# Optimization experiments

Measured on AMD Instinct MI355X. Metric: run time of the kernel, lower is better.

Reference implementation:

```python
import jax, jax.numpy as jnp
import numpy as np

T, B, E, H = 2048, 2, 1024, 16
HD = E // H
EPS = 1e-5


def setup_inputs() -> dict:
    key = jax.random.key(0)
    k1, k2, k3 = jax.random.split(key, 3)
    bound_in = float(np.sqrt(6.0 / (3 * E + E)))   # xavier_uniform for [3E,E]
    bound_out = float(np.sqrt(6.0 / (E + E)))      # xavier_uniform for [E,E]
    return {
        "query": jax.random.normal(k1, (T, B, E), dtype=jnp.float32),
        "gamma": jnp.ones((E,), dtype=jnp.float32),
        "beta": jnp.zeros((E,), dtype=jnp.float32),
        "in_proj_weight": jax.random.uniform(k2, (3 * E, E), jnp.float32, -bound_in, bound_in),
        "out_proj_weight": jax.random.uniform(k3, (E, E), jnp.float32, -bound_out, bound_out),
    }


def reference(query, gamma, beta, in_proj_weight, out_proj_weight):
    # LayerNorm over channel dim
    mean = jnp.mean(query, axis=-1, keepdims=True)
    var = jnp.mean(jnp.square(query - mean), axis=-1, keepdims=True)
    ln = (query - mean) * jax.lax.rsqrt(var + EPS) * gamma + beta  # [T,B,E]

    # Fused QKV projection (no bias): qkv = ln @ W^T, W: [3E, E]
    qkv = jnp.einsum("tbe,fe->tbf", ln, in_proj_weight)  # [T,B,3E]
    q, k, v = jnp.split(qkv, 3, axis=-1)
    q = q.reshape(T, B, H, HD) * (HD ** -0.5)
    k = k.reshape(T, B, H, HD)
    v = v.reshape(T, B, H, HD)

    # Attention: scores [B,H,T,T]
    scores = jnp.einsum("tbhd,sbhd->bhts", q, k)
    attn = jax.nn.softmax(scores, axis=-1)
    ctx = jnp.einsum("bhts,sbhd->tbhd", attn, v).reshape(T, B, E)

    # Output projection + residual add (dropout prob = 0)
    out = jnp.einsum("tbe,fe->tbf", ctx, out_proj_weight)
    return query + out
```

## Files before the change

kernel.cpp:

```cpp
#include <hip/hip_runtime.h>
#include <hip/hip_bf16.h>
#include <math.h>

#define T_DIM 2048
#define B_DIM 2
#define E_DIM 1024
#define H_DIM 16
#define HD_DIM 64
#define M_DIM (T_DIM * B_DIM)
#define BH_DIM (B_DIM * H_DIM)

using bf16x8 = __attribute__((ext_vector_type(8))) __bf16;
using u16x8  = __attribute__((ext_vector_type(8))) unsigned short;
using f32x4  = __attribute__((ext_vector_type(4))) float;

static __device__ __forceinline__ unsigned short f2bf(float f) {
  unsigned u = __builtin_bit_cast(unsigned, f);
  u += 0x7fff + ((u >> 16) & 1);
  return (unsigned short)(u >> 16);
}

__device__ __forceinline__ void gload_lds16(const void* g, void* l) {
  __builtin_amdgcn_global_load_lds(
      (const __attribute__((address_space(1))) unsigned int*)g,
      (__attribute__((address_space(3))) unsigned int*)l, 16, 0, 0);
}

__global__ __launch_bounds__(256) void prep_kernel(
    const float* __restrict__ q, const float* __restrict__ gamma,
    const float* __restrict__ beta, unsigned short* __restrict__ ln_out,
    const float* __restrict__ w1, unsigned short* __restrict__ o1, int n1,
    const float* __restrict__ w2, unsigned short* __restrict__ o2, int n2) {
  int blk = blockIdx.x;
  int tid = threadIdx.x;
  if (blk >= M_DIM) {
    int i = (blk - M_DIM) * 256 + tid;
    const float* in; unsigned short* out; int idx;
    if (i < n1) { in = w1; out = o1; idx = i; }
    else if (i < n1 + n2) { in = w2; out = o2; idx = i - n1; }
    else return;
    float4 v = ((const float4*)in)[idx];
    ushort4 o;
    o.x = f2bf(v.x); o.y = f2bf(v.y); o.z = f2bf(v.z); o.w = f2bf(v.w);
    ((ushort4*)out)[idx] = o;
    return;
  }
  int row = blk;
  const float4* qr = (const float4*)(q + (size_t)row * E_DIM);
  float4 x = qr[tid];
  float s  = x.x + x.y + x.z + x.w;
  float ss = x.x * x.x + x.y * x.y + x.z * x.z + x.w * x.w;
#pragma unroll
  for (int off = 32; off >= 1; off >>= 1) {
    s  += __shfl_xor(s, off, 64);
    ss += __shfl_xor(ss, off, 64);
  }
  __shared__ float red[8];
  int wid = tid >> 6, lane = tid & 63;
  if (lane == 0) { red[wid] = s; red[4 + wid] = ss; }
  __syncthreads();
  s  = red[0] + red[1] + red[2] + red[3];
  ss = red[4] + red[5] + red[6] + red[7];
  float mean = s * (1.0f / E_DIM);
  float var  = ss * (1.0f / E_DIM) - mean * mean;
  float rstd = rsqrtf(var + 1e-5f);
  float4 g4 = ((const float4*)gamma)[tid];
  float4 b4 = ((const float4*)beta)[tid];
  ushort4 o;
  o.x = f2bf((x.x - mean) * rstd * g4.x + b4.x);
  o.y = f2bf((x.y - mean) * rstd * g4.y + b4.y);
  o.z = f2bf((x.z - mean) * rstd * g4.z + b4.z);
  o.w = f2bf((x.w - mean) * rstd * g4.w + b4.w);
  ((ushort4*)(ln_out + (size_t)row * E_DIM))[tid] = o;
}

__global__ __launch_bounds__(256) void gemm0_kernel(
    const unsigned short* __restrict__ A, const unsigned short* __restrict__ Bw,
    unsigned short* __restrict__ out_qkv) {
  __shared__ alignas(16) unsigned short lA[3][128 * 32];
  __shared__ alignas(16) unsigned short lB[3][128 * 32];
  int tid = threadIdx.x;
  int wid = tid >> 6, lane = tid & 63;
  int wm = wid >> 1, wn = wid & 1;
  int g = lane >> 4, lr = lane & 15;
  int m0 = blockIdx.y * 128, n0 = blockIdx.x * 128;
  f32x4 acc[4][4] = {};

  int srcRow[2], srcCol[2];
#pragma unroll
  for (int c = 0; c < 2; ++c) {
    int n = c * 256 + tid;
    int laR = n >> 3, l = (n & 7) ^ (laR & 7);
    srcRow[c] = laR * 2 + (l >> 2);
    srcCol[c] = (l & 3) * 8;
  }
  int rs = (lr >> 1) & 7;
  int fragA = (wm * 32 + (lr >> 1)) * 64 + (((((lr & 1) << 2) | g)) ^ rs) * 8;
  int fragB = (wn * 32 + (lr >> 1)) * 64 + (((((lr & 1) << 2) | g)) ^ rs) * 8;

#define STAGE_G0(BUF, K0)                                                      \
  do {                                                                         \
    _Pragma("unroll")                                                          \
    for (int c = 0; c < 2; ++c) {                                              \
      gload_lds16(A  + (size_t)(m0 + srcRow[c]) * E_DIM + (K0) + srcCol[c],    \
                  lA[BUF] + (size_t)(c * 256 + wid * 64) * 8);                 \
      gload_lds16(Bw + (size_t)(n0 + srcRow[c]) * E_DIM + (K0) + srcCol[c],    \
                  lB[BUF] + (size_t)(c * 256 + wid * 64) * 8);                 \
    }                                                                          \
  } while (0)

#define PROCG0(BUF, NBUF, KK, LAST)                                            \
  do {                                                                         \
    if (!(LAST)) {                                                             \
      STAGE_G0(NBUF, ((KK) + 1) * 32);                                         \
      asm volatile("s_waitcnt vmcnt(4)" ::: "memory");                         \
    } else {                                                                   \
      asm volatile("s_waitcnt vmcnt(0)" ::: "memory");                         \
    }                                                                          \
    __builtin_amdgcn_s_barrier();                                              \
    __builtin_amdgcn_sched_barrier(0);                                         \
    bf16x8 af[4], bfr[4];                                                      \
    _Pragma("unroll")                                                          \
    for (int r = 0; r < 4; ++r) {                                              \
      af[r]  = *(const bf16x8*)(lA[BUF] + fragA + r * 512);                    \
      bfr[r] = *(const bf16x8*)(lB[BUF] + fragB + r * 512);                    \
    }                                                                          \
    __builtin_amdgcn_s_setprio(1);                                             \
    _Pragma("unroll")                                                          \
    for (int mr = 0; mr < 4; ++mr)                                             \
      _Pragma("unroll")                                                        \
      for (int nr = 0; nr < 4; ++nr)                                           \
        acc[mr][nr] = __builtin_amdgcn_mfma_f32_16x16x32_bf16(                 \
            af[mr], bfr[nr], acc[mr][nr], 0, 0, 0);                            \
    __builtin_amdgcn_s_setprio(0);                                             \
  } while (0)

  STAGE_G0(0, 0);
  for (int kk = 0; kk < 30; kk += 3) {
    PROCG0(0, 1, kk + 0, false);
    PROCG0(1, 2, kk + 1, false);
    PROCG0(2, 0, kk + 2, false);
  }
  PROCG0(0, 1, 30, false);
  PROCG0(1, 2, 31, true);
#undef PROCG0
#undef STAGE_G0

#pragma unroll
  for (int mr = 0; mr < 4; ++mr) {
#pragma unroll
    for (int nr = 0; nr < 4; ++nr) {
#pragma unroll
      for (int r = 0; r < 4; ++r) {
        int grow = m0 + wm * 64 + mr * 16 + g * 4 + r;
        int gcol = n0 + wn * 64 + nr * 16 + lr;
        int which = gcol >> 10, rem = gcol & 1023;
        int h = rem >> 6, d = rem & 63;
        int t = grow >> 1, b = grow & 1;
        out_qkv[(size_t)which * (BH_DIM * T_DIM * HD_DIM) +
                ((size_t)(b * H_DIM + h) * T_DIM + t) * HD_DIM + d] =
            f2bf(acc[mr][nr][r]);
      }
    }
  }
}

__global__ __launch_bounds__(256) void gemm1_kernel(
    const unsigned short* __restrict__ A, const unsigned short* __restrict__ Bw,
    const float* __restrict__ resid, float* __restrict__ out) {
  __shared__ alignas(16) unsigned short lA[3][128 * 32];
  __shared__ alignas(16) unsigned short lB[3][64 * 32];
  int tid = threadIdx.x;
  int wid = tid >> 6, lane = tid & 63;
  int g = lane >> 4, lr = lane & 15;
  int m0 = blockIdx.y * 128, n0 = blockIdx.x * 64;
  f32x4 acc[2][4] = {};

  int srcRow[2], srcCol[2];
#pragma unroll
  for (int c = 0; c < 2; ++c) {
    int n = c * 256 + tid;
    int laR = n >> 3, l = (n & 7) ^ (laR & 7);
    srcRow[c] = laR * 2 + (l >> 2);
    srcCol[c] = (l & 3) * 8;
  }
  int rs = (lr >> 1) & 7;
  int physc = ((((lr & 1) << 2) | g)) ^ rs;
  int fragA = (wid * 16 + (lr >> 1)) * 64 + physc * 8;
  int fragB = ((lr >> 1)) * 64 + physc * 8;

#define STAGE_G1(BUF, K0)                                                      \
  do {                                                                         \
    _Pragma("unroll")                                                          \
    for (int c = 0; c < 2; ++c)                                                \
      gload_lds16(A + (size_t)(m0 + srcRow[c]) * E_DIM + (K0) + srcCol[c],     \
                  lA[BUF] + (size_t)(c * 256 + wid * 64) * 8);                 \
    gload_lds16(Bw + (size_t)(n0 + srcRow[0]) * E_DIM + (K0) + srcCol[0],      \
                lB[BUF] + (size_t)(wid * 64) * 8);                             \
  } while (0)

#define PROCG1(BUF, NBUF, KK, LAST)                                            \
  do {                                                                         \
    if (!(LAST)) {                                                             \
      STAGE_G1(NBUF, ((KK) + 1) * 32);                                         \
      asm volatile("s_waitcnt vmcnt(3)" ::: "memory");                         \
    } else {                                                                   \
      asm volatile("s_waitcnt vmcnt(0)" ::: "memory");                         \
    }                                                                          \
    __builtin_amdgcn_s_barrier();                                              \
    __builtin_amdgcn_sched_barrier(0);                                         \
    bf16x8 af[2], bfr[4];                                                      \
    _Pragma("unroll")                                                          \
    for (int r = 0; r < 2; ++r)                                                \
      af[r] = *(const bf16x8*)(lA[BUF] + fragA + r * 512);                     \
    _Pragma("unroll")                                                          \
    for (int r = 0; r < 4; ++r)                                                \
      bfr[r] = *(const bf16x8*)(lB[BUF] + fragB + r * 512);                    \
    __builtin_amdgcn_s_setprio(1);                                             \
    _Pragma("unroll")                                                          \
    for (int mr = 0; mr < 2; ++mr)                                             \
      _Pragma("unroll")                                                        \
      for (int nr = 0; nr < 4; ++nr)                                           \
        acc[mr][nr] = __builtin_amdgcn_mfma_f32_16x16x32_bf16(                 \
            af[mr], bfr[nr], acc[mr][nr], 0, 0, 0);                            \
    __builtin_amdgcn_s_setprio(0);                                             \
  } while (0)

  STAGE_G1(0, 0);
  for (int kk = 0; kk < 30; kk += 3) {
    PROCG1(0, 1, kk + 0, false);
    PROCG1(1, 2, kk + 1, false);
    PROCG1(2, 0, kk + 2, false);
  }
  PROCG1(0, 1, 30, false);
  PROCG1(1, 2, 31, true);
#undef PROCG1
#undef STAGE_G1

#pragma unroll
  for (int mr = 0; mr < 2; ++mr) {
#pragma unroll
    for (int nr = 0; nr < 4; ++nr) {
#pragma unroll
      for (int r = 0; r < 4; ++r) {
        int grow = m0 + wid * 32 + mr * 16 + g * 4 + r;
        int gcol = n0 + nr * 16 + lr;
        size_t idx = (size_t)grow * E_DIM + gcol;
        out[idx] = resid[idx] + acc[mr][nr][r];
      }
    }
  }
}

__global__ __launch_bounds__(256) void transpose_v_kernel(
    const unsigned short* __restrict__ vb, unsigned short* __restrict__ vt) {
  __shared__ alignas(16) unsigned short tl[64 * 72];
  int tid = threadIdx.x;
  int bh = blockIdx.y, t0 = blockIdx.x * 64;
  const unsigned short* src = vb + ((size_t)bh * T_DIM + t0) * HD_DIM;
#pragma unroll
  for (int e = 0; e < 2; ++e) {
    int i8 = e * 256 + tid;
    int r = i8 >> 3;
    int c = (i8 & 7) * 8;
    int hsh = (r ^ (r >> 3)) & 7;
    bf16x8 v = *(const bf16x8*)(src + (size_t)r * HD_DIM + c);
    *(bf16x8*)(tl + r * 72 + (c ^ (hsh << 3))) = v;
  }
  __syncthreads();
  unsigned short* dst = vt + (size_t)bh * HD_DIM * T_DIM + t0;
#pragma unroll
  for (int e = 0; e < 2; ++e) {
    int i8 = e * 256 + tid;
    int d = i8 >> 3;
    int tc = (i8 & 7) * 8;
    u16x8 o;
#pragma unroll
    for (int j = 0; j < 8; ++j) {
      int p = tc + j;
      int ks = p >> 5, gg = (p >> 3) & 3, jl = p & 7;
      int r = (ks * 2 + (jl >> 2)) * 16 + gg * 4 + (jl & 3);
      int hsh = (r ^ (r >> 3)) & 7;
      o[j] = tl[r * 72 + (d ^ (hsh << 3))];
    }
    *(u16x8*)(dst + (size_t)d * T_DIM + tc) = o;
  }
}

__global__ __launch_bounds__(256) void attn_kernel(
    const unsigned short* __restrict__ qb, const unsigned short* __restrict__ kb,
    const unsigned short* __restrict__ vt, unsigned short* __restrict__ ctx) {
  __shared__ alignas(16) unsigned short lK[4][64 * 64];
  __shared__ alignas(16) unsigned short lV[4][64 * 64];
  int tid = threadIdx.x;
  int wid = tid >> 6, lane = tid & 63;
  int g = lane >> 4, lr = lane & 15;
  int f = blockIdx.x;
  int xcd = f & 7, rest = f >> 3;
  int bh = xcd + 8 * (rest & 3);
  int qt = rest >> 2;
  int b = bh >> 4, h = bh & 15;
  const size_t koff = (size_t)bh * T_DIM * HD_DIM;
  const size_t voff = (size_t)bh * HD_DIM * T_DIM;

  int srow = tid >> 3;
  int gch  = (tid & 7) ^ (srow & 7);
  const unsigned short* ks0 = kb + koff + (size_t)srow * HD_DIM + gch * 8;
  const unsigned short* vs0 = vt + voff + (size_t)srow * T_DIM + gch * 8;

#define STAGE_TILE(buf, T)                                                     \
  do {                                                                         \
    size_t kofs = (size_t)(T) * 64 * HD_DIM;                                   \
    size_t vofs = (size_t)(T) * 64;                                            \
    gload_lds16(ks0 + kofs,                 lK[buf] + wid * 512);              \
    gload_lds16(ks0 + kofs + 32 * HD_DIM,   lK[buf] + 2048 + wid * 512);       \
    gload_lds16(vs0 + vofs,                 lV[buf] + wid * 512);              \
    gload_lds16(vs0 + vofs + (size_t)32 * T_DIM, lV[buf] + 2048 + wid * 512);  \
  } while (0)

  bf16x8 qf[2][2];
  {
    const float QS = 0.125f * 1.44269504f;
#pragma unroll
    for (int qa = 0; qa < 2; ++qa) {
      int qrow = qt * 128 + wid * 32 + qa * 16 + lr;
#pragma unroll
      for (int ks = 0; ks < 2; ++ks) {
        bf16x8 raw = *(const bf16x8*)(qb + koff + (size_t)qrow * HD_DIM + ks * 32 + g * 8);
#pragma unroll
        for (int j = 0; j < 8; ++j) qf[qa][ks][j] = (__bf16)((float)raw[j] * QS);
      }
    }
  }

  bf16x8 onesf;
#pragma unroll
  for (int j = 0; j < 8; ++j) onesf[j] = (__bf16)1.0f;

  f32x4 accO[2][4] = {};
  f32x4 accS[2] = {};

#define COMPUTE_TILE(B)                                                        \
  do {                                                                         \
    const unsigned short* Kc = lK[B];                                          \
    const unsigned short* Vc = lV[B];                                          \
    f32x4 s4[2][4];                                                            \
    __builtin_amdgcn_s_setprio(1);                                             \
    _Pragma("unroll")                                                          \
    for (int cf = 0; cf < 4; ++cf) {                                           \
      int row = cf * 16 + lr;                                                  \
      int sw = (row & 7) << 3;                                                 \
      bf16x8 k0 = *(const bf16x8*)(Kc + row * 64 + ((g * 8) ^ sw));            \
      bf16x8 k1 = *(const bf16x8*)(Kc + row * 64 + ((32 + g * 8) ^ sw));       \
      _Pragma("unroll")                                                        \
      for (int qa = 0; qa < 2; ++qa) {                                         \
        f32x4 s = {-8.0f, -8.0f, -8.0f, -8.0f};                                \
        s = __builtin_amdgcn_mfma_f32_16x16x32_bf16(k0, qf[qa][0], s, 0, 0, 0);\
        s = __builtin_amdgcn_mfma_f32_16x16x32_bf16(k1, qf[qa][1], s, 0, 0, 0);\
        s4[qa][cf] = s;                                                        \
      }                                                                        \
    }                                                                          \
    __builtin_amdgcn_s_setprio(0);                                             \
    bf16x8 pf[2][2];                                                           \
    _Pragma("unroll")                                                          \
    for (int qa = 0; qa < 2; ++qa)                                             \
      _Pragma("unroll")                                                        \
      for (int j = 0; j < 8; ++j) {                                            \
        pf[qa][0][j] = (__bf16)__builtin_amdgcn_exp2f(s4[qa][(j >> 2)][j & 3]);\
        pf[qa][1][j] = (__bf16)__builtin_amdgcn_exp2f(s4[qa][2 + (j >> 2)][j & 3]);\
      }                                                                        \
    __builtin_amdgcn_s_setprio(1);                                             \
    _Pragma("unroll")                                                          \
    for (int ks = 0; ks < 2; ++ks) {                                           \
      _Pragma("unroll")                                                        \
      for (int qa = 0; qa < 2; ++qa)                                           \
        accS[qa] = __builtin_amdgcn_mfma_f32_16x16x32_bf16(onesf, pf[qa][ks], accS[qa], 0, 0, 0); \
      _Pragma("unroll")                                                        \
      for (int df = 0; df < 4; ++df) {                                         \
        int row = df * 16 + lr;                                                \
        int sw = (row & 7) << 3;                                               \
        bf16x8 vf = *(const bf16x8*)(Vc + row * 64 + ((ks * 32 + g * 8) ^ sw));\
        _Pragma("unroll")                                                      \
        for (int qa = 0; qa < 2; ++qa)                                         \
          accO[qa][df] = __builtin_amdgcn_mfma_f32_16x16x32_bf16(vf, pf[qa][ks], accO[qa][df], 0, 0, 0); \
      }                                                                        \
    }                                                                          \
    __builtin_amdgcn_s_setprio(0);                                             \
  } while (0)

#define INTERVAL(BA, BB, SA, SB, TT, STG)                                      \
  do {                                                                         \
    asm volatile("s_waitcnt vmcnt(0)" ::: "memory");                           \
    __builtin_amdgcn_s_barrier();                                              \
    __builtin_amdgcn_sched_barrier(0);                                         \
    if (STG) {                                                                 \
      STAGE_TILE(SA, (TT) + 2);                                                \
      STAGE_TILE(SB, (TT) + 3);                                                \
    }                                                                          \
    COMPUTE_TILE(BA);                                                          \
    COMPUTE_TILE(BB);                                                          \
  } while (0)

  STAGE_TILE(0, 0);
  STAGE_TILE(1, 1);
  for (int tt = 0; tt < 28; tt += 4) {
    INTERVAL(0, 1, 2, 3, tt, true);
    INTERVAL(2, 3, 0, 1, tt + 2, true);
  }
  INTERVAL(0, 1, 2, 3, 28, true);
  INTERVAL(2, 3, 0, 1, 30, false);
#undef INTERVAL
#undef COMPUTE_TILE
#undef STAGE_TILE

  __syncthreads();
  unsigned short* sc = (unsigned short*)lK + wid * (32 * 72);
  float invl[2];
  invl[0] = 1.0f / accS[0][0];
  invl[1] = 1.0f / accS[1][0];
#pragma unroll
  for (int qa = 0; qa < 2; ++qa)
#pragma unroll
    for (int df = 0; df < 4; ++df)
#pragma unroll
      for (int r = 0; r < 4; ++r)
        sc[(qa * 16 + lr) * 72 + df * 16 + g * 4 + r] =
            f2bf(accO[qa][df][r] * invl[qa]);
  __syncthreads();
#pragma unroll
  for (int i = 0; i < 4; ++i) {
    int idx = i * 64 + lane;
    int row = idx >> 3, ch = idx & 7;
    u16x8 v8 = *(const u16x8*)(sc + row * 72 + ch * 8);
    int t = qt * 128 + wid * 32 + row;
    *(u16x8*)(&ctx[((size_t)t * B_DIM + b) * E_DIM + h * HD_DIM + ch * 8]) = v8;
  }
}

extern "C" void kernel_launch(void* const* d_in, const int* in_sizes, int n_in,
                              void* d_out, int out_size, void* d_ws, size_t ws_size,
                              hipStream_t stream) {
  const float* query = (const float*)d_in[0];
  const float* gamma = (const float*)d_in[1];
  const float* beta  = (const float*)d_in[2];
  const float* w_in  = (const float*)d_in[3];
  const float* w_out = (const float*)d_in[4];
  float* out = (float*)d_out;

  unsigned short* ws    = (unsigned short*)d_ws;
  unsigned short* ln    = ws;
  unsigned short* winb  = ln + (size_t)M_DIM * E_DIM;
  unsigned short* woutb = winb + (size_t)3 * E_DIM * E_DIM;
  unsigned short* qkv   = woutb + (size_t)E_DIM * E_DIM;

  unsigned short* qbuf = qkv;
  unsigned short* kbuf = qkv + (size_t)BH_DIM * T_DIM * HD_DIM;
  unsigned short* vbuf = kbuf + (size_t)BH_DIM * T_DIM * HD_DIM;
  unsigned short* vtb  = ln;
  unsigned short* ctx  = vbuf;

  prep_kernel<<<dim3(M_DIM + 4096), dim3(256), 0, stream>>>(
      query, gamma, beta, ln,
      w_in, winb, 3 * E_DIM * E_DIM / 4, w_out, woutb, E_DIM * E_DIM / 4);
  gemm0_kernel<<<dim3(3 * E_DIM / 128, M_DIM / 128), dim3(256), 0, stream>>>(
      ln, winb, qkv);
  transpose_v_kernel<<<dim3(T_DIM / 64, BH_DIM), dim3(256), 0, stream>>>(vbuf, vtb);
  attn_kernel<<<dim3(512), dim3(256), 0, stream>>>(qbuf, kbuf, vtb, ctx);
  gemm1_kernel<<<dim3(E_DIM / 64, M_DIM / 128), dim3(256), 0, stream>>>(
      ctx, woutb, query, out);
}
```

Measured before the change: 122.1 us.

## Restructure QKV GEMM into 256x256 tiles with 8 waves and phased pipelining

The QKV projection GEMM moves from 128x128 tiles with 4 waves and a K-step of 32 to 256x256 tiles with 8 waves and a K-step of 64. Loads into a 128KB LDS double buffer are split into half-tile stages interleaved across four compute phases. The aim is more operand reuse per LDS load and better overlap of global loads with MFMA work. In exchange, the grid shrinks to 192 blocks, fewer than the CU count, so occupancy and wave parallelism drop, and each thread holds more registers.

After: 113.9 us. 1.07x faster.

```diff
diff --git a/kernel.cpp b/kernel.cpp
--- a/kernel.cpp
+++ b/kernel.cpp
@@ -74,92 +74,125 @@
   ((ushort4*)(ln_out + (size_t)row * E_DIM))[tid] = o;
 }
 
-__global__ __launch_bounds__(256) void gemm0_kernel(
+__global__ __launch_bounds__(512) void gemm0_kernel(
     const unsigned short* __restrict__ A, const unsigned short* __restrict__ Bw,
     unsigned short* __restrict__ out_qkv) {
-  __shared__ alignas(16) unsigned short lA[3][128 * 32];
-  __shared__ alignas(16) unsigned short lB[3][128 * 32];
+  __shared__ alignas(16) unsigned short lds[65536];
   int tid = threadIdx.x;
   int wid = tid >> 6, lane = tid & 63;
-  int wm = wid >> 1, wn = wid & 1;
+  int wm = wid >> 2, wn = wid & 3;
   int g = lane >> 4, lr = lane & 15;
-  int m0 = blockIdx.y * 128, n0 = blockIdx.x * 128;
-  f32x4 acc[4][4] = {};
-
-  int srcRow[2], srcCol[2];
-#pragma unroll
-  for (int c = 0; c < 2; ++c) {
-    int n = c * 256 + tid;
-    int laR = n >> 3, l = (n & 7) ^ (laR & 7);
-    srcRow[c] = laR * 2 + (l >> 2);
-    srcCol[c] = (l & 3) * 8;
-  }
-  int rs = (lr >> 1) & 7;
-  int fragA = (wm * 32 + (lr >> 1)) * 64 + (((((lr & 1) << 2) | g)) ^ rs) * 8;
-  int fragB = (wn * 32 + (lr >> 1)) * 64 + (((((lr & 1) << 2) | g)) ^ rs) * 8;
-
-#define STAGE_G0(BUF, K0)                                                      \
-  do {                                                                         \
-    _Pragma("unroll")                                                          \
-    for (int c = 0; c < 2; ++c) {                                              \
-      gload_lds16(A  + (size_t)(m0 + srcRow[c]) * E_DIM + (K0) + srcCol[c],    \
-                  lA[BUF] + (size_t)(c * 256 + wid * 64) * 8);                 \
-      gload_lds16(Bw + (size_t)(n0 + srcRow[c]) * E_DIM + (K0) + srcCol[c],    \
-                  lB[BUF] + (size_t)(c * 256 + wid * 64) * 8);                 \
+  int m0 = blockIdx.y * 256, n0 = blockIdx.x * 256;
+  f32x4 acc[8][4] = {};
+  bf16x8 bfr[4][2];
+
+  int srl  = tid >> 3;
+  int scol = ((tid & 7) ^ (srl & 7)) * 8;
+  int koff0 = ((0 * 4 + g) ^ (lr & 7)) * 8;
+  int koff1 = ((1 * 4 + g) ^ (lr & 7)) * 8;
+  int bhalf = wn >> 1;
+  int brow  = (wn & 1) * 64;
+
+#define STAGE_HALF(PTR, GR0, KT, LBASE)                                        \
+  do {                                                                         \
+    gload_lds16((PTR) + (size_t)((GR0) + srl) * E_DIM + (size_t)(KT) * 64 + scol, \
+                lds + (LBASE) + (size_t)tid * 8);                              \
+    gload_lds16((PTR) + (size_t)((GR0) + 64 + srl) * E_DIM + (size_t)(KT) * 64 + scol, \
+                lds + (LBASE) + 4096 + (size_t)tid * 8);                       \
+  } while (0)
+
+#define AOFF(D, MR, KK) (((D) * 2 + wm) * 8192 + ((MR) * 16 + lr) * 64 + ((KK) ? koff1 : koff0))
+#define BOFF(D, NF, KK) (32768 + ((D) * 2 + bhalf) * 8192 + (brow + (NF) * 16 + lr) * 64 + ((KK) ? koff1 : koff0))
+
+#define PHASE(Q, D, DOB, VW, ...)                                              \
+  do {                                                                         \
+    bf16x8 af[2][2];                                                           \
+    _Pragma("unroll")                                                          \
+    for (int mi = 0; mi < 2; ++mi) {                                           \
+      af[mi][0] = *(const bf16x8*)(lds + AOFF(D, 2 * (Q) + mi, 0));            \
+      af[mi][1] = *(const bf16x8*)(lds + AOFF(D, 2 * (Q) + mi, 1));            \
     }                                                                          \
-  } while (0)
-
-#define PROCG0(BUF, NBUF, KK, LAST)                                            \
-  do {                                                                         \
-    if (!(LAST)) {                                                             \
-      STAGE_G0(NBUF, ((KK) + 1) * 32);                                         \
-      asm volatile("s_waitcnt vmcnt(4)" ::: "memory");                         \
-    } else {                                                                   \
-      asm volatile("s_waitcnt vmcnt(0)" ::: "memory");                         \
+    if (DOB) {                                                                 \
+      _Pragma("unroll")                                                        \
+      for (int nf = 0; nf < 4; ++nf) {                                         \
+        bfr[nf][0] = *(const bf16x8*)(lds + BOFF(D, nf, 0));                   \
+        bfr[nf][1] = *(const bf16x8*)(lds + BOFF(D, nf, 1));                   \
+      }                                                                        \
     }                                                                          \
+    __VA_ARGS__;                                                               \
+    VW;                                                                        \
     __builtin_amdgcn_s_barrier();                                              \
     __builtin_amdgcn_sched_barrier(0);                                         \
-    bf16x8 af[4], bfr[4];                                                      \
-    _Pragma("unroll")                                                          \
-    for (int r = 0; r < 4; ++r) {                                              \
-      af[r]  = *(const bf16x8*)(lA[BUF] + fragA + r * 512);                    \
-      bfr[r] = *(const bf16x8*)(lB[BUF] + fragB + r * 512);                    \
-    }                                                                          \
     __builtin_amdgcn_s_setprio(1);                                             \
     _Pragma("unroll")                                                          \
-    for (int mr = 0; mr < 4; ++mr)                                             \
-      _Pragma("unroll")                                                        \
-      for (int nr = 0; nr < 4; ++nr)                                           \
-        acc[mr][nr] = __builtin_amdgcn_mfma_f32_16x16x32_bf16(                 \
-            af[mr], bfr[nr], acc[mr][nr], 0, 0, 0);                            \
+    for (int mi = 0; mi < 2; ++mi)                                             \
+      _Pragma("unroll")                                                        \
+      for (int nf = 0; nf < 4; ++nf) {                                         \
+        acc[2 * (Q) + mi][nf] = __builtin_amdgcn_mfma_f32_16x16x32_bf16(       \
+            af[mi][0], bfr[nf][0], acc[2 * (Q) + mi][nf], 0, 0, 0);            \
+        acc[2 * (Q) + mi][nf] = __builtin_amdgcn_mfma_f32_16x16x32_bf16(       \
+            af[mi][1], bfr[nf][1], acc[2 * (Q) + mi][nf], 0, 0, 0);            \
+      }                                                                        \
     __builtin_amdgcn_s_setprio(0);                                             \
-  } while (0)
-
-  STAGE_G0(0, 0);
-  for (int kk = 0; kk < 30; kk += 3) {
-    PROCG0(0, 1, kk + 0, false);
-    PROCG0(1, 2, kk + 1, false);
-    PROCG0(2, 0, kk + 2, false);
-  }
-  PROCG0(0, 1, 30, false);
-  PROCG0(1, 2, 31, true);
-#undef PROCG0
-#undef STAGE_G0
-
-#pragma unroll
-  for (int mr = 0; mr < 4; ++mr) {
-#pragma unroll
-    for (int nr = 0; nr < 4; ++nr) {
+    __builtin_amdgcn_s_barrier();                                              \
+    __builtin_amdgcn_sched_barrier(0);                                         \
+  } while (0)
+
+#define VMC4 asm volatile("s_waitcnt vmcnt(4)" ::: "memory")
+#define VMC0 asm volatile("s_waitcnt vmcnt(0)" ::: "memory")
+#define NOWAIT ((void)0)
+
+  STAGE_HALF(Bw, n0,       0, 32768);
+  STAGE_HALF(Bw, n0 + 128, 0, 40960);
+  STAGE_HALF(A,  m0,       0, 0);
+  STAGE_HALF(A,  m0 + 128, 0, 8192);
+  STAGE_HALF(Bw, n0,       1, 49152);
+  STAGE_HALF(Bw, n0 + 128, 1, 57344);
+  VMC0;
+  __builtin_amdgcn_s_barrier();
+  __builtin_amdgcn_sched_barrier(0);
+
+  for (int i = 0; i < 7; ++i) {
+    int k1 = 2 * i + 1, k2 = 2 * i + 2, k3 = 2 * i + 3;
+    PHASE(0, 0, true,  NOWAIT, STAGE_HALF(A,  m0,       k1, 16384));
+    PHASE(1, 0, false, NOWAIT, STAGE_HALF(A,  m0 + 128, k1, 24576));
+    PHASE(2, 0, false, NOWAIT, STAGE_HALF(Bw, n0,       k2, 32768));
+    PHASE(3, 0, false, VMC4,   STAGE_HALF(Bw, n0 + 128, k2, 40960));
+    PHASE(0, 1, true,  NOWAIT, STAGE_HALF(A,  m0,       k2, 0));
+    PHASE(1, 1, false, NOWAIT, STAGE_HALF(A,  m0 + 128, k2, 8192));
+    PHASE(2, 1, false, NOWAIT, STAGE_HALF(Bw, n0,       k3, 49152));
+    PHASE(3, 1, false, VMC4,   STAGE_HALF(Bw, n0 + 128, k3, 57344));
+  }
+  PHASE(0, 0, true,  NOWAIT, STAGE_HALF(A,  m0,       15, 16384));
+  PHASE(1, 0, false, NOWAIT, STAGE_HALF(A,  m0 + 128, 15, 24576));
+  PHASE(2, 0, false, NOWAIT, );
+  PHASE(3, 0, false, VMC0,   );
+  PHASE(0, 1, true,  NOWAIT, );
+  PHASE(1, 1, false, NOWAIT, );
+  PHASE(2, 1, false, NOWAIT, );
+  PHASE(3, 1, false, NOWAIT, );
+#undef PHASE
+#undef STAGE_HALF
+#undef AOFF
+#undef BOFF
+#undef VMC4
+#undef VMC0
+#undef NOWAIT
+
+#pragma unroll
+  for (int mr = 0; mr < 8; ++mr) {
+#pragma unroll
+    for (int nf = 0; nf < 4; ++nf) {
 #pragma unroll
       for (int r = 0; r < 4; ++r) {
-        int grow = m0 + wm * 64 + mr * 16 + g * 4 + r;
-        int gcol = n0 + wn * 64 + nr * 16 + lr;
+        int grow = m0 + wm * 128 + mr * 16 + g * 4 + r;
+        int gcol = n0 + wn * 64 + nf * 16 + lr;
         int which = gcol >> 10, rem = gcol & 1023;
         int h = rem >> 6, d = rem & 63;
         int t = grow >> 1, b = grow & 1;
         out_qkv[(size_t)which * (BH_DIM * T_DIM * HD_DIM) +
                 ((size_t)(b * H_DIM + h) * T_DIM + t) * HD_DIM + d] =
-            f2bf(acc[mr][nr][r]);
+            f2bf(acc[mr][nf][r]);
       }
     }
   }
@@ -462,7 +495,7 @@
   prep_kernel<<<dim3(M_DIM + 4096), dim3(256), 0, stream>>>(
       query, gamma, beta, ln,
       w_in, winb, 3 * E_DIM * E_DIM / 4, w_out, woutb, E_DIM * E_DIM / 4);
-  gemm0_kernel<<<dim3(3 * E_DIM / 128, M_DIM / 128), dim3(256), 0, stream>>>(
+  gemm0_kernel<<<dim3(3 * E_DIM / 256, M_DIM / 256), dim3(512), 0, stream>>>(
       ln, winb, qkv);
   transpose_v_kernel<<<dim3(T_DIM / 64, BH_DIM), dim3(256), 0, stream>>>(vbuf, vtb);
   attn_kernel<<<dim3(512), dim3(256), 0, stream>>>(qbuf, kbuf, vtb, ctx);
```
